# Kernel tuning notes

Hardware: AMD Instinct MI355X
Metric: run time of the kernel (lower is better)

## Reference

```python
import jax, jax.numpy as jnp
import numpy as np

# Config constants (match init_kwargs)
N_EXPERTS = 8
CAPACITY = 1280
W_IMPORTANCE = 0.01
W_LOAD = 0.01
LAMBDA_Z = 0.001
W_PENALTY = 0.01


def setup_inputs() -> dict:
    key = jax.random.key(0)
    ks = jax.random.split(key, 6)
    B, T, C, E, F = 4, 2048, 1024, N_EXPERTS, 4096
    s = 0.02
    return {
        "x": jax.random.normal(ks[0], (B, T, C), dtype=jnp.float32),
        "gate_w": jax.random.normal(ks[1], (E, C), dtype=jnp.float32) * s,
        "gate_b": jnp.zeros((E,), dtype=jnp.float32),
        "w1": jax.random.normal(ks[2], (E, F, C), dtype=jnp.float32) * s,
        "b1": jnp.zeros((E, F), dtype=jnp.float32),
        "w2": jax.random.normal(ks[3], (E, C, F), dtype=jnp.float32) * s,
        "b2": jnp.zeros((E, C), dtype=jnp.float32),
    }


def reference(x, gate_w, gate_b, w1, b1, w2, b2):
    B, T, C = x.shape
    E = N_EXPERTS
    xf = x.reshape(B * T, C)
    bt = xf.shape[0]

    # ---- routing ----
    gate_logits = xf @ gate_w.T + gate_b  # (BT, E)

    # penalty loss
    p = jax.nn.softmax(gate_logits / 1.66, axis=-1)
    pen_a = jnp.mean(p * (1.0 - p))
    pm = p.mean(axis=0)
    pen_b = 1.0 / E - jnp.mean(pm * (1.0 - pm))
    penalty = W_PENALTY * (pen_a + pen_b)

    # z-loss
    z_loss = LAMBDA_Z * jnp.mean(jax.nn.logsumexp(gate_logits, axis=-1) ** 2)

    router_probs = jax.nn.softmax(gate_logits.astype(jnp.float32), axis=-1).astype(x.dtype)
    top1_idx = jnp.argmax(router_probs, axis=-1)        # (BT,)
    top1_w = jnp.max(router_probs, axis=-1)             # (BT,)
    onehot = jax.nn.one_hot(top1_idx, E, dtype=jnp.int32)

    # capacity masking: position of each token within its chosen expert
    priority = jnp.cumsum(onehot, axis=0)               # (BT, E)
    pos = priority[jnp.arange(bt), top1_idx] - 1        # (BT,)
    keep = pos < CAPACITY                               # (BT,) bool

    # load-balance loss
    f_i = onehot.astype(x.dtype).mean(axis=0)
    P_i = router_probs.mean(axis=0)
    load_loss = W_LOAD * E * jnp.sum(f_i * P_i)

    # importance loss (scatter of top1 probs == onehot-weighted sum)
    importance = (onehot.astype(x.dtype) * top1_w[:, None]).sum(axis=0)  # (E,)
    cv2 = jnp.var(importance) / jnp.mean(importance) ** 2
    importance_loss = W_IMPORTANCE * cv2

    aux_loss = penalty + z_loss + load_loss + importance_loss

    # ---- dispatch -> grouped FFN -> combine ----
    pos_c = jnp.clip(pos, 0, CAPACITY - 1)
    keep_f = keep.astype(x.dtype)[:, None]
    buf = jnp.zeros((E, CAPACITY, C), dtype=x.dtype).at[top1_idx, pos_c].add(xf * keep_f)
    h = jax.nn.gelu(jnp.einsum('ekc,efc->ekf', buf, w1) + b1[:, None, :], approximate=True)
    yb = jnp.einsum('ekf,ecf->ekc', h, w2) + b2[:, None, :]
    y = yb[top1_idx, pos_c] * keep_f                    # dropped tokens -> 0

    out = (top1_w[:, None] * y).reshape(B, T, C)
    return out, aux_loss
```

## Files before the change

kernel.cpp:

```cpp
#include <hip/hip_runtime.h>
#include <hip/hip_bf16.h>
#include <stdint.h>

#define BTOK 8192
#define CDIM 1024
#define NEXP 8
#define FDIM 4096
#define ECAP 1280
#define NGB (BTOK / 4)

typedef __attribute__((ext_vector_type(8))) unsigned short u16x8;
typedef __attribute__((ext_vector_type(8))) __bf16 bf16x8;
typedef __attribute__((ext_vector_type(4))) float f32x4;

#define WAIT_VM8()  asm volatile("s_waitcnt vmcnt(8)" ::: "memory")
#define WAIT_VM0()  asm volatile("s_waitcnt vmcnt(0)" ::: "memory")
#define BARSCHED()  do { __builtin_amdgcn_s_barrier(); __builtin_amdgcn_sched_barrier(0); } while (0)

__device__ __forceinline__ unsigned short f2bf(float f) {
    unsigned int u = __builtin_bit_cast(unsigned int, f);
    u += 0x7FFFu + ((u >> 16) & 1u);
    return (unsigned short)(u >> 16);
}

__device__ __forceinline__ bf16x8 lds_load8(const unsigned short* p) {
    return __builtin_bit_cast(bf16x8, *(const u16x8*)p);
}

__device__ __forceinline__ float gelu_tanh(float v) {
    float u = 0.7978845608028654f * (v + 0.044715f * v * v * v);
    float e = __expf(2.0f * u);
    float t = 1.0f - 2.0f * __builtin_amdgcn_rcpf(e + 1.0f);
    return 0.5f * v * (1.0f + t);
}

__device__ __forceinline__ void glds16(const unsigned short* g, unsigned short* l) {
    __builtin_amdgcn_global_load_lds(
        (const __attribute__((address_space(1))) void*)g,
        (__attribute__((address_space(3))) void*)l,
        16, 0, 0);
}

__device__ __forceinline__ void stage_tile(
    const unsigned short* const* gA, const unsigned short* const* gB,
    unsigned short* As, unsigned short* Bs, int wbase, int koff)
{
#pragma unroll
    for (int j = 0; j < 4; j++) {
        glds16(gA[j] + koff, As + j * 2048 + wbase);
        glds16(gB[j] + koff, Bs + j * 2048 + wbase);
    }
}

__device__ __forceinline__ void mfma_tile(
    const unsigned short* As, const unsigned short* Bs,
    int wm, int wn, int fr, int kq, int sw, f32x4 acc[4][4])
{
#pragma unroll
    for (int kk = 0; kk < 64; kk += 32) {
        bf16x8 af[4], bfr[4];
#pragma unroll
        for (int i = 0; i < 4; i++) {
            af[i]  = lds_load8(&As[(wm * 64 + i * 16 + fr) * 64 + ((kk + kq) ^ sw)]);
            bfr[i] = lds_load8(&Bs[(wn * 64 + i * 16 + fr) * 64 + ((kk + kq) ^ sw)]);
        }
#pragma unroll
        for (int i = 0; i < 4; i++)
#pragma unroll
            for (int j = 0; j < 4; j++)
                acc[i][j] = __builtin_amdgcn_mfma_f32_16x16x32_bf16(af[i], bfr[j], acc[i][j], 0, 0, 0);
    }
}

__global__ __launch_bounds__(256) void cvtw_kernel(
    const float* __restrict__ w1, const float* __restrict__ w2,
    unsigned short* __restrict__ d1, unsigned short* __restrict__ d2, int n8)
{
    const float* src = blockIdx.y ? w2 : w1;
    unsigned short* dst = blockIdx.y ? d2 : d1;
    int i = blockIdx.x * 256 + threadIdx.x;
    if (i >= n8) return;
    const float4* s = (const float4*)(src + (size_t)i * 8);
    float4 a = s[0], b = s[1];
    u16x8 o;
    o[0] = f2bf(a.x); o[1] = f2bf(a.y); o[2] = f2bf(a.z); o[3] = f2bf(a.w);
    o[4] = f2bf(b.x); o[5] = f2bf(b.y); o[6] = f2bf(b.z); o[7] = f2bf(b.w);
    *(u16x8*)(dst + (size_t)i * 8) = o;
}

__global__ __launch_bounds__(256) void gate_kernel(
    const float* __restrict__ x,
    const float* __restrict__ gw,
    const float* __restrict__ gb,
    unsigned short* __restrict__ xb,
    int* __restrict__ top1i, float* __restrict__ top1w,
    float* __restrict__ partials)
{
    const int lane = threadIdx.x & 63;
    const int wave = threadIdx.x >> 6;
    const int tok = blockIdx.x * 4 + wave;
    const float* xr = x + (size_t)tok * CDIM + lane * 16;
    float xv[16];
#pragma unroll
    for (int j = 0; j < 4; j++) {
        float4 v = ((const float4*)xr)[j];
        xv[4 * j] = v.x; xv[4 * j + 1] = v.y; xv[4 * j + 2] = v.z; xv[4 * j + 3] = v.w;
    }
    u16x8 o0, o1;
#pragma unroll
    for (int j = 0; j < 8; j++) o0[j] = f2bf(xv[j]);
#pragma unroll
    for (int j = 0; j < 8; j++) o1[j] = f2bf(xv[8 + j]);
    unsigned short* xo = xb + (size_t)tok * CDIM + lane * 16;
    *(u16x8*)xo = o0;
    *(u16x8*)(xo + 8) = o1;

    float acc[8];
#pragma unroll
    for (int e = 0; e < 8; e++) {
        const float* wr = gw + e * CDIM + lane * 16;
        float s = 0.f;
#pragma unroll
        for (int j = 0; j < 4; j++) {
            float4 v = ((const float4*)wr)[j];
            s += xv[4 * j] * v.x + xv[4 * j + 1] * v.y + xv[4 * j + 2] * v.z + xv[4 * j + 3] * v.w;
        }
        acc[e] = s;
    }
#pragma unroll
    for (int e = 0; e < 8; e++) {
#pragma unroll
        for (int off = 32; off > 0; off >>= 1)
            acc[e] += __shfl_xor(acc[e], off);
    }
    const float INV_T = 1.0f / 1.66f;
    float l[8];
#pragma unroll
    for (int e = 0; e < 8; e++) l[e] = acc[e] + gb[e];
    float m = l[0];
#pragma unroll
    for (int e = 1; e < 8; e++) m = fmaxf(m, l[e]);
    float ex[8], se = 0.f;
#pragma unroll
    for (int e = 0; e < 8; e++) { ex[e] = __expf(l[e] - m); se += ex[e]; }
    float inv = 1.0f / se;
    int am = 0; float bl = l[0];
#pragma unroll
    for (int e = 1; e < 8; e++) if (l[e] > bl) { bl = l[e]; am = e; }
    float w = ex[am] * inv;
    float lse = m + __logf(se);
    float zz = lse * lse;
    float m2 = m * INV_T, se2 = 0.f, ex2[8];
#pragma unroll
    for (int e = 0; e < 8; e++) { ex2[e] = __expf(l[e] * INV_T - m2); se2 += ex2[e]; }
    float inv2 = 1.0f / se2;
    float pen = 0.f, q[8];
#pragma unroll
    for (int e = 0; e < 8; e++) { q[e] = ex2[e] * inv2; pen += q[e] * (1.f - q[e]); }

    __shared__ float part[26][4];
    if (lane == 0) {
        top1i[tok] = am;
        top1w[tok] = w;
        part[0][wave] = pen;
        part[1][wave] = zz;
#pragma unroll
        for (int e = 0; e < 8; e++) {
            part[2 + e][wave]  = q[e];
            part[10 + e][wave] = ex[e] * inv;
            part[18 + e][wave] = (e == am) ? w : 0.f;
        }
    }
    __syncthreads();
    const int tid = threadIdx.x;
    if (tid < 26)
        partials[tid * NGB + blockIdx.x] =
            part[tid][0] + part[tid][1] + part[tid][2] + part[tid][3];
}

__global__ __launch_bounds__(256) void route_kernel(
    const int* __restrict__ top1i, const float* __restrict__ top1w,
    const float* __restrict__ partials,
    int* __restrict__ toks, float* __restrict__ slotw,
    int* __restrict__ cnt, float* __restrict__ aux_out)
{
    const int tid = threadIdx.x;
    const int TPT = BTOK / 256;
    int ti[TPT];
    int cnte[8] = {};
#pragma unroll
    for (int i = 0; i < TPT; i++) {
        ti[i] = top1i[tid * TPT + i];
#pragma unroll
        for (int e = 0; e < 8; e++) cnte[e] += (ti[i] == e) ? 1 : 0;
    }

    __shared__ int sc[256][8];
#pragma unroll
    for (int e = 0; e < 8; e++) sc[tid][e] = cnte[e];
    __syncthreads();
    for (int st = 1; st < 256; st <<= 1) {
        int v[8];
        bool act = (tid >= st);
        if (act) {
#pragma unroll
            for (int e = 0; e < 8; e++) v[e] = sc[tid - st][e];
        }
        __syncthreads();
        if (act) {
#pragma unroll
            for (int e = 0; e < 8; e++) sc[tid][e] += v[e];
        }
        __syncthreads();
    }
    int run[8], tot[8];
#pragma unroll
    for (int e = 0; e < 8; e++) {
        run[e] = (tid > 0) ? sc[tid - 1][e] : 0;
        tot[e] = sc[255][e];
    }
#pragma unroll
    for (int i = 0; i < TPT; i++) {
        int t = tid * TPT + i;
        int am = ti[i];
        int pos = 0;
#pragma unroll
        for (int e = 0; e < 8; e++) if (e == am) pos = run[e]++;
        if (pos < ECAP) {
            toks[am * ECAP + pos] = t;
            slotw[am * ECAP + pos] = top1w[t];
        }
    }
    if (tid < 8) cnt[tid] = (tot[tid] < ECAP) ? tot[tid] : ECAP;

    float r[26];
#pragma unroll
    for (int j = 0; j < 26; j++) {
        float s = 0.f;
        for (int i = tid; i < NGB; i += 256) s += partials[j * NGB + i];
        r[j] = s;
    }
    __shared__ float red[26][256];
#pragma unroll
    for (int j = 0; j < 26; j++) red[j][tid] = r[j];
    __syncthreads();
    for (int st = 128; st > 0; st >>= 1) {
        if (tid < st) {
#pragma unroll
            for (int j = 0; j < 26; j++) red[j][tid] += red[j][tid + st];
        }
        __syncthreads();
    }
    if (tid == 0) {
        const float BTf = (float)BTOK;
        float pen_a = red[0][0] / (BTf * 8.f);
        float pb = 0.f;
        for (int e = 0; e < 8; e++) { float pm = red[2 + e][0] / BTf; pb += pm * (1.f - pm); }
        float pen_b = 0.125f - pb * 0.125f;
        float penalty = 0.01f * (pen_a + pen_b);
        float z = 0.001f * red[1][0] / BTf;
        float load = 0.f;
        for (int e = 0; e < 8; e++) load += ((float)tot[e] / BTf) * (red[10 + e][0] / BTf);
        load *= 0.01f * 8.f;
        float mu = 0.f;
        for (int e = 0; e < 8; e++) mu += red[18 + e][0];
        mu *= 0.125f;
        float var = 0.f;
        for (int e = 0; e < 8; e++) { float d = red[18 + e][0] - mu; var += d * d; }
        var *= 0.125f;
        float cv2 = var / (mu * mu);
        float aux = penalty + z + load + 0.01f * cv2;
        aux_out[0] = aux;
    }
}

__global__ __launch_bounds__(256) void ffn1_kernel(
    const unsigned short* __restrict__ xb,
    const unsigned short* __restrict__ w1b,
    const float* __restrict__ b1,
    const int* __restrict__ toks,
    const int* __restrict__ cnt,
    unsigned short* __restrict__ H)
{
    const int e = blockIdx.y;
    const int MT = ECAP / 128;
    const int nbq = (int)gridDim.x >> 3;
    const int bid = blockIdx.x;
    const int b2 = (bid & 7) * nbq + (bid >> 3);
    const int mt = b2 % MT;
    const int nt = b2 / MT;
    const int cnt_e = cnt[e];
    const int m0 = mt * 128;
    if (m0 >= cnt_e) return;
    const int n0 = nt * 128;
    const unsigned short* W = w1b + (size_t)e * FDIM * CDIM;
    const int* tk = toks + e * ECAP;

    __shared__ __align__(16) unsigned short As[2 * 128 * 64];
    __shared__ __align__(16) unsigned short Bs[2 * 128 * 64];

    const int tid = threadIdx.x;
    const int lane = tid & 63;
    const int wave = tid >> 6;
    const int wm = wave & 1;
    const int wn = wave >> 1;
    const int wbase = wave * 512;

    const unsigned short* gA[4];
    const unsigned short* gB[4];
#pragma unroll
    for (int j = 0; j < 4; j++) {
        int idx = j * 256 + tid;
        int r = idx >> 3;
        int ch = (idx & 7) ^ (r & 7);
        int row = m0 + r;
        int tokid = (row < cnt_e) ? tk[row] : 0;
        if ((unsigned)tokid >= BTOK) tokid = 0;
        gA[j] = xb + (size_t)tokid * CDIM + ch * 8;
        gB[j] = W + (size_t)(n0 + r) * CDIM + ch * 8;
    }
    f32x4 acc[4][4] = {};
    const int fr = lane & 15;
    const int kq = (lane >> 4) * 8;
    const int sw = (fr & 7) << 3;

    stage_tile(gA, gB, As, Bs, wbase, 0);
    WAIT_VM0();
    BARSCHED();

    const int NT = CDIM / 64;
#pragma unroll 1
    for (int t = 0; t < NT; t += 2) {
        stage_tile(gA, gB, As + 8192, Bs + 8192, wbase, (t + 1) * 64);
        WAIT_VM8();
        BARSCHED();
        mfma_tile(As, Bs, wm, wn, fr, kq, sw, acc);
        BARSCHED();
        if (t + 2 < NT) {
            stage_tile(gA, gB, As, Bs, wbase, (t + 2) * 64);
            WAIT_VM8();
        } else {
            WAIT_VM0();
        }
        BARSCHED();
        mfma_tile(As + 8192, Bs + 8192, wm, wn, fr, kq, sw, acc);
        BARSCHED();
    }
    const int cq = (lane >> 4) * 4;
#pragma unroll
    for (int i = 0; i < 4; i++) {
#pragma unroll
        for (int j = 0; j < 4; j++) {
            int n = n0 + wn * 64 + j * 16 + fr;
            float bias = b1[e * FDIM + n];
            size_t base = ((size_t)e * ECAP + (m0 + wm * 64 + i * 16 + cq)) * FDIM + n;
#pragma unroll
            for (int rr = 0; rr < 4; rr++) {
                float v = acc[i][j][rr] + bias;
                H[base + (size_t)rr * FDIM] = f2bf(gelu_tanh(v));
            }
        }
    }
}

__global__ __launch_bounds__(256) void ffn2_kernel(
    const unsigned short* __restrict__ H,
    const unsigned short* __restrict__ w2b,
    const float* __restrict__ b2,
    const int* __restrict__ toks,
    const float* __restrict__ slotw,
    const int* __restrict__ cnt,
    float* __restrict__ out)
{
    const int e = blockIdx.y;
    const int MT = ECAP / 128;
    const int nbq = (int)gridDim.x >> 3;
    const int bid = blockIdx.x;
    const int b2i = (bid & 7) * nbq + (bid >> 3);
    const int mt = b2i % MT;
    const int nt = b2i / MT;
    const int cnt_e = cnt[e];
    const int m0 = mt * 128;
    if (m0 >= cnt_e) return;
    const int n0 = nt * 128;
    const unsigned short* W = w2b + (size_t)e * CDIM * FDIM;
    const unsigned short* Hb = H + (size_t)e * ECAP * FDIM;

    __shared__ __align__(16) unsigned short As[2 * 128 * 64];
    __shared__ __align__(16) unsigned short Bs[2 * 128 * 64];

    const int tid = threadIdx.x;
    const int lane = tid & 63;
    const int wave = tid >> 6;
    const int wm = wave & 1;
    const int wn = wave >> 1;
    const int wbase = wave * 512;

    const unsigned short* gA[4];
    const unsigned short* gB[4];
#pragma unroll
    for (int j = 0; j < 4; j++) {
        int idx = j * 256 + tid;
        int r = idx >> 3;
        int ch = (idx & 7) ^ (r & 7);
        gA[j] = Hb + (size_t)(m0 + r) * FDIM + ch * 8;
        gB[j] = W + (size_t)(n0 + r) * FDIM + ch * 8;
    }
    f32x4 acc[4][4] = {};
    const int fr = lane & 15;
    const int kq = (lane >> 4) * 8;
    const int sw = (fr & 7) << 3;

    stage_tile(gA, gB, As, Bs, wbase, 0);
    WAIT_VM0();
    BARSCHED();

    const int NT = FDIM / 64;
#pragma unroll 1
    for (int t = 0; t < NT; t += 2) {
        stage_tile(gA, gB, As + 8192, Bs + 8192, wbase, (t + 1) * 64);
        WAIT_VM8();
        BARSCHED();
        mfma_tile(As, Bs, wm, wn, fr, kq, sw, acc);
        BARSCHED();
        if (t + 2 < NT) {
            stage_tile(gA, gB, As, Bs, wbase, (t + 2) * 64);
            WAIT_VM8();
        } else {
            WAIT_VM0();
        }
        BARSCHED();
        mfma_tile(As + 8192, Bs + 8192, wm, wn, fr, kq, sw, acc);
        BARSCHED();
    }
    const int cq = (lane >> 4) * 4;
#pragma unroll
    for (int i = 0; i < 4; i++) {
#pragma unroll
        for (int rr = 0; rr < 4; rr++) {
            int s = m0 + wm * 64 + i * 16 + cq + rr;
            if (s < cnt_e) {
                int t = toks[e * ECAP + s];
                float wgt = slotw[e * ECAP + s];
                if ((unsigned)t < BTOK) {
#pragma unroll
                    for (int j = 0; j < 4; j++) {
                        int n = n0 + wn * 64 + j * 16 + fr;
                        float y = acc[i][j][rr] + b2[e * CDIM + n];
                        out[(size_t)t * CDIM + n] = wgt * y;
                    }
                }
            }
        }
    }
}

extern "C" void kernel_launch(void* const* d_in, const int* in_sizes, int n_in,
                              void* d_out, int out_size, void* d_ws, size_t ws_size,
                              hipStream_t stream)
{
    (void)in_sizes; (void)n_in; (void)ws_size;
    const float* x  = (const float*)d_in[0];
    const float* gw = (const float*)d_in[1];
    const float* gb = (const float*)d_in[2];
    const float* w1 = (const float*)d_in[3];
    const float* b1 = (const float*)d_in[4];
    const float* w2 = (const float*)d_in[5];
    const float* b2 = (const float*)d_in[6];
    float* out = (float*)d_out;

    char* ws = (char*)d_ws;
    size_t off = 0;
    unsigned short* H   = (unsigned short*)(ws + off); off += (size_t)NEXP * ECAP * FDIM * 2;
    unsigned short* xb  = (unsigned short*)(ws + off); off += (size_t)BTOK * CDIM * 2;
    unsigned short* w1b = (unsigned short*)(ws + off); off += (size_t)NEXP * FDIM * CDIM * 2;
    unsigned short* w2b = (unsigned short*)(ws + off); off += (size_t)NEXP * CDIM * FDIM * 2;
    float* partials = (float*)(ws + off); off += (size_t)26 * NGB * 4;
    int* top1i    = (int*)(ws + off);   off += (size_t)BTOK * 4;
    float* top1w  = (float*)(ws + off); off += (size_t)BTOK * 4;
    int* toks     = (int*)(ws + off);   off += (size_t)NEXP * ECAP * 4;
    float* slotw  = (float*)(ws + off); off += (size_t)NEXP * ECAP * 4;
    int* cnt      = (int*)(ws + off);   off += (size_t)NEXP * 4;

    hipMemsetAsync(d_out, 0, (size_t)out_size * sizeof(float), stream);

    const int NW = NEXP * FDIM * CDIM / 8;
    cvtw_kernel<<<dim3((NW + 255) / 256, 2), 256, 0, stream>>>(w1, w2, w1b, w2b, NW);

    gate_kernel<<<NGB, 256, 0, stream>>>(x, gw, gb, xb, top1i, top1w, partials);
    route_kernel<<<1, 256, 0, stream>>>(top1i, top1w, partials, toks, slotw, cnt,
                                        out + (size_t)BTOK * CDIM);
    ffn1_kernel<<<dim3((ECAP / 128) * (FDIM / 128), NEXP), 256, 0, stream>>>(xb, w1b, b1, toks, cnt, H);
    ffn2_kernel<<<dim3((ECAP / 128) * (CDIM / 128), NEXP), 256, 0, stream>>>(H, w2b, b2, toks, slotw, cnt, out);
}
```

Before: 693.3 us.

## Fuse fp32-to-bf16 weight conversion into FFN GEMM B-tile staging

Removes the separate weight conversion kernel and its bf16 weight buffers. Both FFN GEMMs now load fp32 weight tiles into registers, convert them to bf16 and write them to LDS, while activation tiles keep using direct global-to-LDS loads. Wait counts are retuned and MFMA priority is raised during compute. This avoids a full read and write pass over both weight tensors, but the GEMMs now read twice the weight bytes per tile reuse and carry extra register pressure and conversion ALU work.

```diff
diff --git a/kernel.cpp b/kernel.cpp
--- a/kernel.cpp
+++ b/kernel.cpp
@@ -13,8 +13,11 @@
 typedef __attribute__((ext_vector_type(8))) __bf16 bf16x8;
 typedef __attribute__((ext_vector_type(4))) float f32x4;
 
-#define WAIT_VM8()  asm volatile("s_waitcnt vmcnt(8)" ::: "memory")
+#define WAIT_VM12() asm volatile("s_waitcnt vmcnt(12)" ::: "memory")
+#define WAIT_VM4()  asm volatile("s_waitcnt vmcnt(4)" ::: "memory")
 #define WAIT_VM0()  asm volatile("s_waitcnt vmcnt(0)" ::: "memory")
+#define WAIT_LGKM0() asm volatile("s_waitcnt lgkmcnt(0)" ::: "memory")
+#define SCHED_FENCE() __builtin_amdgcn_sched_barrier(0)
 #define BARSCHED()  do { __builtin_amdgcn_s_barrier(); __builtin_amdgcn_sched_barrier(0); } while (0)
 
 __device__ __forceinline__ unsigned short f2bf(float f) {
@@ -41,14 +44,32 @@
         16, 0, 0);
 }
 
-__device__ __forceinline__ void stage_tile(
-    const unsigned short* const* gA, const unsigned short* const* gB,
-    unsigned short* As, unsigned short* Bs, int wbase, int koff)
+__device__ __forceinline__ void stage_A(const unsigned short* const* gA,
+                                        unsigned short* As, int wbase, int koff)
+{
+#pragma unroll
+    for (int j = 0; j < 4; j++) glds16(gA[j] + koff, As + j * 2048 + wbase);
+}
+
+__device__ __forceinline__ void loadB(const float* const* gBf, int koff, float4* bv)
 {
 #pragma unroll
     for (int j = 0; j < 4; j++) {
-        glds16(gA[j] + koff, As + j * 2048 + wbase);
-        glds16(gB[j] + koff, Bs + j * 2048 + wbase);
+        const float4* p = (const float4*)(gBf[j] + koff);
+        bv[2 * j]     = p[0];
+        bv[2 * j + 1] = p[1];
+    }
+}
+
+__device__ __forceinline__ void writeB(const float4* bv, unsigned short* Bs, int tid)
+{
+#pragma unroll
+    for (int j = 0; j < 4; j++) {
+        float4 a = bv[2 * j], b = bv[2 * j + 1];
+        u16x8 o;
+        o[0] = f2bf(a.x); o[1] = f2bf(a.y); o[2] = f2bf(a.z); o[3] = f2bf(a.w);
+        o[4] = f2bf(b.x); o[5] = f2bf(b.y); o[6] = f2bf(b.z); o[7] = f2bf(b.w);
+        *(u16x8*)(Bs + j * 2048 + tid * 8) = o;
     }
 }
 
@@ -72,20 +93,34 @@
     }
 }
 
-__global__ __launch_bounds__(256) void cvtw_kernel(
-    const float* __restrict__ w1, const float* __restrict__ w2,
-    unsigned short* __restrict__ d1, unsigned short* __restrict__ d2, int n8)
-{
-    const float* src = blockIdx.y ? w2 : w1;
-    unsigned short* dst = blockIdx.y ? d2 : d1;
-    int i = blockIdx.x * 256 + threadIdx.x;
-    if (i >= n8) return;
-    const float4* s = (const float4*)(src + (size_t)i * 8);
-    float4 a = s[0], b = s[1];
-    u16x8 o;
-    o[0] = f2bf(a.x); o[1] = f2bf(a.y); o[2] = f2bf(a.z); o[3] = f2bf(a.w);
-    o[4] = f2bf(b.x); o[5] = f2bf(b.y); o[6] = f2bf(b.z); o[7] = f2bf(b.w);
-    *(u16x8*)(dst + (size_t)i * 8) = o;
+__device__ __forceinline__ void ffn_phase(
+    const unsigned short* const* gA, const float* const* gBf,
+    const unsigned short* CA, const unsigned short* CB,
+    unsigned short* NA, unsigned short* NB,
+    int wbase, int tid, int koff_next, bool has_next,
+    int wm, int wn, int fr, int kq, int sw, f32x4 acc[4][4])
+{
+    float4 bv[8];
+    if (has_next) {
+        loadB(gBf, koff_next, bv);
+        SCHED_FENCE();
+        stage_A(gA, NA, wbase, koff_next);
+        SCHED_FENCE();
+        WAIT_VM12();
+    } else {
+        WAIT_VM0();
+    }
+    BARSCHED();
+    __builtin_amdgcn_s_setprio(1);
+    mfma_tile(CA, CB, wm, wn, fr, kq, sw, acc);
+    __builtin_amdgcn_s_setprio(0);
+    if (has_next) {
+        WAIT_VM4();
+        SCHED_FENCE();
+        writeB(bv, NB, tid);
+        WAIT_LGKM0();
+    }
+    BARSCHED();
 }
 
 __global__ __launch_bounds__(256) void gate_kernel(
@@ -276,7 +311,7 @@
 
 __global__ __launch_bounds__(256) void ffn1_kernel(
     const unsigned short* __restrict__ xb,
-    const unsigned short* __restrict__ w1b,
+    const float* __restrict__ w1,
     const float* __restrict__ b1,
     const int* __restrict__ toks,
     const int* __restrict__ cnt,
@@ -293,7 +328,7 @@
     const int m0 = mt * 128;
     if (m0 >= cnt_e) return;
     const int n0 = nt * 128;
-    const unsigned short* W = w1b + (size_t)e * FDIM * CDIM;
+    const float* Wf = w1 + (size_t)e * FDIM * CDIM;
     const int* tk = toks + e * ECAP;
 
     __shared__ __align__(16) unsigned short As[2 * 128 * 64];
@@ -307,7 +342,7 @@
     const int wbase = wave * 512;
 
     const unsigned short* gA[4];
-    const unsigned short* gB[4];
+    const float* gBf[4];
 #pragma unroll
     for (int j = 0; j < 4; j++) {
         int idx = j * 256 + tid;
@@ -317,34 +352,35 @@
         int tokid = (row < cnt_e) ? tk[row] : 0;
         if ((unsigned)tokid >= BTOK) tokid = 0;
         gA[j] = xb + (size_t)tokid * CDIM + ch * 8;
-        gB[j] = W + (size_t)(n0 + r) * CDIM + ch * 8;
+        gBf[j] = Wf + (size_t)(n0 + r) * CDIM + ch * 8;
     }
     f32x4 acc[4][4] = {};
     const int fr = lane & 15;
     const int kq = (lane >> 4) * 8;
     const int sw = (fr & 7) << 3;
 
-    stage_tile(gA, gB, As, Bs, wbase, 0);
-    WAIT_VM0();
-    BARSCHED();
+    {
+        float4 bv[8];
+        loadB(gBf, 0, bv);
+        SCHED_FENCE();
+        stage_A(gA, As, wbase, 0);
+        SCHED_FENCE();
+        WAIT_VM4();
+        writeB(bv, Bs, tid);
+        WAIT_VM0();
+        WAIT_LGKM0();
+        BARSCHED();
+    }
 
     const int NT = CDIM / 64;
 #pragma unroll 1
     for (int t = 0; t < NT; t += 2) {
-        stage_tile(gA, gB, As + 8192, Bs + 8192, wbase, (t + 1) * 64);
-        WAIT_VM8();
-        BARSCHED();
-        mfma_tile(As, Bs, wm, wn, fr, kq, sw, acc);
-        BARSCHED();
-        if (t + 2 < NT) {
-            stage_tile(gA, gB, As, Bs, wbase, (t + 2) * 64);
-            WAIT_VM8();
-        } else {
-            WAIT_VM0();
-        }
-        BARSCHED();
-        mfma_tile(As + 8192, Bs + 8192, wm, wn, fr, kq, sw, acc);
-        BARSCHED();
+        ffn_phase(gA, gBf, As, Bs, As + 8192, Bs + 8192,
+                  wbase, tid, (t + 1) * 64, true,
+                  wm, wn, fr, kq, sw, acc);
+        ffn_phase(gA, gBf, As + 8192, Bs + 8192, As, Bs,
+                  wbase, tid, (t + 2) * 64, (t + 2 < NT),
+                  wm, wn, fr, kq, sw, acc);
     }
     const int cq = (lane >> 4) * 4;
 #pragma unroll
@@ -365,7 +401,7 @@
 
 __global__ __launch_bounds__(256) void ffn2_kernel(
     const unsigned short* __restrict__ H,
-    const unsigned short* __restrict__ w2b,
+    const float* __restrict__ w2,
     const float* __restrict__ b2,
     const int* __restrict__ toks,
     const float* __restrict__ slotw,
@@ -383,7 +419,7 @@
     const int m0 = mt * 128;
     if (m0 >= cnt_e) return;
     const int n0 = nt * 128;
-    const unsigned short* W = w2b + (size_t)e * CDIM * FDIM;
+    const float* Wf = w2 + (size_t)e * CDIM * FDIM;
     const unsigned short* Hb = H + (size_t)e * ECAP * FDIM;
 
     __shared__ __align__(16) unsigned short As[2 * 128 * 64];
@@ -397,41 +433,42 @@
     const int wbase = wave * 512;
 
     const unsigned short* gA[4];
-    const unsigned short* gB[4];
+    const float* gBf[4];
 #pragma unroll
     for (int j = 0; j < 4; j++) {
         int idx = j * 256 + tid;
         int r = idx >> 3;
         int ch = (idx & 7) ^ (r & 7);
         gA[j] = Hb + (size_t)(m0 + r) * FDIM + ch * 8;
-        gB[j] = W + (size_t)(n0 + r) * FDIM + ch * 8;
+        gBf[j] = Wf + (size_t)(n0 + r) * FDIM + ch * 8;
     }
     f32x4 acc[4][4] = {};
     const int fr = lane & 15;
     const int kq = (lane >> 4) * 8;
     const int sw = (fr & 7) << 3;
 
-    stage_tile(gA, gB, As, Bs, wbase, 0);
-    WAIT_VM0();
-    BARSCHED();
+    {
+        float4 bv[8];
+        loadB(gBf, 0, bv);
+        SCHED_FENCE();
+        stage_A(gA, As, wbase, 0);
+        SCHED_FENCE();
+        WAIT_VM4();
+        writeB(bv, Bs, tid);
+        WAIT_VM0();
+        WAIT_LGKM0();
+        BARSCHED();
+    }
 
     const int NT = FDIM / 64;
 #pragma unroll 1
     for (int t = 0; t < NT; t += 2) {
-        stage_tile(gA, gB, As + 8192, Bs + 8192, wbase, (t + 1) * 64);
-        WAIT_VM8();
-        BARSCHED();
-        mfma_tile(As, Bs, wm, wn, fr, kq, sw, acc);
-        BARSCHED();
-        if (t + 2 < NT) {
-            stage_tile(gA, gB, As, Bs, wbase, (t + 2) * 64);
-            WAIT_VM8();
-        } else {
-            WAIT_VM0();
-        }
-        BARSCHED();
-        mfma_tile(As + 8192, Bs + 8192, wm, wn, fr, kq, sw, acc);
-        BARSCHED();
+        ffn_phase(gA, gBf, As, Bs, As + 8192, Bs + 8192,
+                  wbase, tid, (t + 1) * 64, true,
+                  wm, wn, fr, kq, sw, acc);
+        ffn_phase(gA, gBf, As + 8192, Bs + 8192, As, Bs,
+                  wbase, tid, (t + 2) * 64, (t + 2 < NT),
+                  wm, wn, fr, kq, sw, acc);
     }
     const int cq = (lane >> 4) * 4;
 #pragma unroll
@@ -473,8 +510,6 @@
     size_t off = 0;
     unsigned short* H   = (unsigned short*)(ws + off); off += (size_t)NEXP * ECAP * FDIM * 2;
     unsigned short* xb  = (unsigned short*)(ws + off); off += (size_t)BTOK * CDIM * 2;
-    unsigned short* w1b = (unsigned short*)(ws + off); off += (size_t)NEXP * FDIM * CDIM * 2;
-    unsigned short* w2b = (unsigned short*)(ws + off); off += (size_t)NEXP * CDIM * FDIM * 2;
     float* partials = (float*)(ws + off); off += (size_t)26 * NGB * 4;
     int* top1i    = (int*)(ws + off);   off += (size_t)BTOK * 4;
     float* top1w  = (float*)(ws + off); off += (size_t)BTOK * 4;
@@ -484,12 +519,9 @@
 
     hipMemsetAsync(d_out, 0, (size_t)out_size * sizeof(float), stream);
 
-    const int NW = NEXP * FDIM * CDIM / 8;
-    cvtw_kernel<<<dim3((NW + 255) / 256, 2), 256, 0, stream>>>(w1, w2, w1b, w2b, NW);
-
     gate_kernel<<<NGB, 256, 0, stream>>>(x, gw, gb, xb, top1i, top1w, partials);
     route_kernel<<<1, 256, 0, stream>>>(top1i, top1w, partials, toks, slotw, cnt,
                                         out + (size_t)BTOK * CDIM);
-    ffn1_kernel<<<dim3((ECAP / 128) * (FDIM / 128), NEXP), 256, 0, stream>>>(xb, w1b, b1, toks, cnt, H);
-    ffn2_kernel<<<dim3((ECAP / 128) * (CDIM / 128), NEXP), 256, 0, stream>>>(H, w2b, b2, toks, slotw, cnt, out);
-}
+    ffn1_kernel<<<dim3((ECAP / 128) * (FDIM / 128), NEXP), 256, 0, stream>>>(xb, w1, b1, toks, cnt, H);
+    ffn2_kernel<<<dim3((ECAP / 128) * (CDIM / 128), NEXP), 256, 0, stream>>>(H, w2, b2, toks, slotw, cnt, out);
+}
```

Result: slower. 741.2 us (+6.9%).
